# Performance work log

Measured on AMD Instinct MI355X. Metric: run time of the kernel, lower is better.

The kernel has to match this reference:

```python
import jax, jax.numpy as jnp
import numpy as np

B, F = 512, 300  # F must satisfy F+4 == 16*19
EPS = 1e-5

def _leaky(v):
    return jnp.where(v >= 0, v, 0.01 * v)

def setup_inputs() -> dict:
    key = jax.random.key(0)
    ks = jax.random.split(key, 9)
    def conv_w(k, o, i):
        return jax.random.normal(k, (o, i), dtype=jnp.float32) * (1.0 / np.sqrt(i))
    x = jax.random.uniform(ks[0], (B, F), dtype=jnp.float32)
    return {
        "x": x,
        "w1": conv_w(ks[1], 256, 512), "b1": jnp.zeros((256,), jnp.float32),
        "w2": conv_w(ks[2], 128, 256), "b2": jnp.zeros((128,), jnp.float32),
        "w3": conv_w(ks[3], 64, 128),  "b3": jnp.zeros((64,), jnp.float32),
        "w4": conv_w(ks[4], 4, 64),    "b4": jnp.zeros((4,), jnp.float32),
    }

def reference(x, w1, b1, w2, b2, w3, b3, w4, b4):
    b = x.shape[0]
    xp = jnp.pad(x, ((0, 0), (2, 2)))                       # (b, 304)
    s1 = xp[:, None, :]                                      # unsqueeze(1)
    s2 = xp[:, :, None]                                      # unsqueeze(2)
    DI = s1 - s2                                             # (b,304,304)
    NDI = DI / (s1 + s2 + EPS)
    t = jnp.stack([DI, NDI], axis=-1)                        # (b,304,304,2)
    # tile into 16x16 grid of 19x19 patches, concat patches along channel
    # channel c = (row*16+col)*2 + d  (row-major loop order in original)
    t = t.reshape(b, 16, 19, 16, 19, 2).transpose(0, 2, 4, 1, 3, 5).reshape(b, 19, 19, 512)
    h = _leaky(jnp.einsum('bhwc,oc->bhwo', t, w1) + b1)      # (b,19,19,256)
    h = _leaky(jnp.einsum('bhwc,oc->bhwo', h, w2) + b2)      # (b,19,19,128)
    # masking branch (positional encoding in original is dead code / overwritten)
    m = jax.nn.relu(jnp.einsum('bhwc,oc->bhwo', h, w3) + b3)  # (b,19,19,64)
    m = jax.nn.relu(jnp.einsum('bhwc,oc->bhwo', m, w4) + b4)  # (b,19,19,4)
    m = m.transpose(3, 0, 1, 2).reshape(4, b, 19 * 19)
    m = jax.nn.softmax(m, axis=2).reshape(4, b, 19, 19, 1)
    # split 128 channels into 4 groups of 32
    g = h.reshape(b, 19, 19, 4, 32).transpose(3, 0, 1, 2, 4)  # (4,b,19,19,32)
    out = (g * m).sum(axis=(2, 3))                            # (4,b,32)
    return out.transpose(1, 0, 2).reshape(b, 128)
```

## Files before the change

kernel.cpp:

```cpp
#include <hip/hip_runtime.h>
#include <math.h>

typedef unsigned short ushort_t;
typedef __attribute__((ext_vector_type(8))) short short8;
typedef __attribute__((ext_vector_type(4))) float f32x4;

#define NTILES 12

#define WS_W_USHORTS 115712

__device__ inline ushort_t f2bf(float f) {
    unsigned u = __float_as_uint(f);
    return (ushort_t)((u + 0x7FFFu + ((u >> 16) & 1u)) >> 16);
}
__device__ inline unsigned pkbf(float f0, float f1) {
    unsigned a = __float_as_uint(f0) + 0x8000u;
    unsigned b = __float_as_uint(f1) + 0x8000u;
    return __builtin_amdgcn_perm(b, a, 0x07060302u);
}
__device__ inline float leaky(float v) { return fmaxf(v, 0.01f * v); }

__global__ void pack_weights(const float* __restrict__ w1, const float* __restrict__ w2,
                             const float* __restrict__ w3, const float* __restrict__ w4,
                             ushort_t* __restrict__ ws) {
    const int idx = blockIdx.x * 256 + threadIdx.x;
    if (idx >= WS_W_USHORTS) return;
    float val = 0.f;
    if (idx < 73728) {
        const int j = idx & 7, lane = (idx >> 3) & 63, blk = idx >> 9;
        const int ks = blk % 9, os = blk / 9;
        const int m = lane & 15, q = lane >> 4;
        const int row = os * 16 + m;
        if (ks < 8) {
            const int k = ks * 32 + q * 8 + j;
            const int i1 = k >> 4, j1 = k & 15;
            val = w1[row * 512 + i1 * 32 + j1 * 2 + 1];
        } else {
            const int sub = q * 8 + j;
            if (sub < 16) {
                const int j1 = sub;
                float s = 0.f;
                #pragma unroll
                for (int i1 = 0; i1 < 16; ++i1) s += w1[row * 512 + i1 * 32 + j1 * 2];
                val = s;
            } else {
                const int i1 = sub - 16;
                float s = 0.f;
                #pragma unroll
                for (int j1 = 0; j1 < 16; ++j1) s += w1[row * 512 + i1 * 32 + j1 * 2];
                val = -s;
            }
        }
    } else if (idx < 106496) {
        const int l = idx - 73728;
        const int j = l & 7, lane = (l >> 3) & 63, blk = l >> 9;
        const int ks = blk & 7, os = blk >> 3;
        const int m = lane & 15, q = lane >> 4;
        val = w2[(os * 16 + m) * 256 + ks * 32 + q * 8 + j];
    } else if (idx < 114688) {
        const int l = idx - 106496;
        const int j = l & 7, lane = (l >> 3) & 63, blk = l >> 9;
        const int ks = blk & 3, os = blk >> 2;
        const int m = lane & 15, q = lane >> 4;
        val = w3[(os * 16 + m) * 128 + ks * 32 + q * 8 + j];
    } else {
        const int l = idx - 114688;
        const int j = l & 7, lane = (l >> 3) & 63, ks = l >> 9;
        const int m = lane & 15, q = lane >> 4;
        val = (m < 4) ? w4[m * 64 + ks * 32 + q * 8 + j] : 0.f;
    }
    ws[idx] = f2bf(val);
}

template <int NS>
__global__ __launch_bounds__(256, 3) void fused_mfma(
    const float* __restrict__ x, const ushort_t* __restrict__ ws,
    const float* __restrict__ b1, const float* __restrict__ b2,
    const float* __restrict__ b3, const float* __restrict__ b4,
    float* __restrict__ partA, float* __restrict__ partS)
{
    __shared__ __align__(16) ushort_t sm[19048];
    ushort_t* const ts   = sm;
    ushort_t* const h2s  = sm;
    ushort_t* const h1s  = sm + 10240;
    ushort_t* const m3s  = sm + 10240;
    float*   const ebuf  = (float*)(sm + 12288);
    float*   const xp    = (float*)(sm + 18432);

    constexpr int SH  = (NS == 4) ? 2 : ((NS == 2) ? 1 : 0);
    constexpr int TPS = (NTILES + NS - 1) / NS;
    const int tid = threadIdx.x;
    const int s   = blockIdx.x & (NS - 1);
    const int bb  = blockIdx.x >> SH;
    const int t0  = s * TPS;
    const int t1  = (t0 + TPS < NTILES) ? (t0 + TPS) : NTILES;

    const int wid  = tid >> 6;
    const int lane = tid & 63;
    const int n0   = lane & 15;
    const int qi   = lane >> 4;
    const int sx   = n0 & 7;
    const int row0 = qi * 4;

    for (int jj = tid; jj < 308; jj += 256) {
        float v = 0.f;
        const int src = jj - 2;
        if (src >= 0 && src < 300) v = x[bb * 300 + src];
        xp[jj] = v;
    }

    const short8* wf1 = (const short8*)(ws);
    const short8* wf2 = (const short8*)(ws + 73728);
    const short8* wf3 = (const short8*)(ws + 106496);
    const short8* wf4 = (const short8*)(ws + 114688);

    f32x4 bv1[4], bv2[2], bv3, bv4;
    #pragma unroll
    for (int jo = 0; jo < 4; ++jo) bv1[jo] = *(const f32x4*)&b1[(wid * 4 + jo) * 16 + row0];
    #pragma unroll
    for (int jo = 0; jo < 2; ++jo) bv2[jo] = *(const f32x4*)&b2[(wid * 2 + jo) * 16 + row0];
    bv3 = *(const f32x4*)&b3[wid * 16 + row0];
    bv4 = *(const f32x4*)&b4[0];

    f32x4 Afr[2] = {{0.f, 0.f, 0.f, 0.f}, {0.f, 0.f, 0.f, 0.f}};
    float Ss = 0.f;

    __syncthreads();

    for (int tile = t0; tile < t1; ++tile) {
        const int pos0 = tile * 32;

        {
            const int p   = tid & 31;
            const int i1b = tid >> 5;
            int posg = pos0 + p; if (posg > 360) posg = 360;
            const int hh = posg / 19;
            const int ww = posg - 19 * hh;
            const int base = p * 320;
            const int psw  = p & 7;
            float u[16];
            #pragma unroll
            for (int j1 = 0; j1 < 16; ++j1) u[j1] = xp[j1 * 19 + ww];
            #pragma unroll
            for (int ii = 0; ii < 2; ++ii) {
                const int i1 = i1b + ii * 8;
                const float v = xp[i1 * 19 + hh];
                #pragma unroll
                for (int j1 = 0; j1 < 16; j1 += 2) {
                    const float nd0 = (u[j1] - v)     * __builtin_amdgcn_rcpf(u[j1] + v + 1e-5f);
                    const float nd1 = (u[j1 + 1] - v) * __builtin_amdgcn_rcpf(u[j1 + 1] + v + 1e-5f);
                    const int oct = i1 * 2 + (j1 >> 3);
                    *(unsigned*)&ts[base + ((oct ^ psw) << 3) + (j1 & 7)] = pkbf(nd0, nd1);
                }
            }
            if (i1b == 0) {
                #pragma unroll
                for (int j1 = 0; j1 < 16; j1 += 2) {
                    const int oct = 32 + (j1 >> 3);
                    *(unsigned*)&ts[base + ((oct ^ psw) << 3) + (j1 & 7)] = pkbf(u[j1], u[j1 + 1]);
                }
                #pragma unroll
                for (int i1 = 0; i1 < 16; i1 += 2) {
                    const float v0 = xp[i1 * 19 + hh];
                    const float v1 = xp[(i1 + 1) * 19 + hh];
                    const int oct = 34 + (i1 >> 3);
                    *(unsigned*)&ts[base + ((oct ^ psw) << 3) + (i1 & 7)] = pkbf(v0, v1);
                }
            }
        }
        __syncthreads();

        {
            f32x4 acc[4][2];
            #pragma unroll
            for (int jo = 0; jo < 4; ++jo) { acc[jo][0] = bv1[jo]; acc[jo][1] = bv1[jo]; }
            const int tb0 = n0 * 320;
            const int tb1 = tb0 + 16 * 320;
            const int wbase = wid * 2304 + lane;
            #pragma unroll 3
            for (int ks = 0; ks < 9; ++ks) {
                const int oct = ks * 4 + qi;
                const short8 bb0 = *(const short8*)&ts[tb0 + ((oct ^ sx) << 3)];
                const short8 bb1 = *(const short8*)&ts[tb1 + ((oct ^ sx) << 3)];
                #pragma unroll
                for (int jo = 0; jo < 4; ++jo) {
                    const short8 a = wf1[wbase + (jo * 9 + ks) * 64];
                    acc[jo][0] = __builtin_amdgcn_mfma_f32_16x16x32_bf16(a, bb0, acc[jo][0], 0, 0, 0);
                    acc[jo][1] = __builtin_amdgcn_mfma_f32_16x16x32_bf16(a, bb1, acc[jo][1], 0, 0, 0);
                }
            }
            #pragma unroll
            for (int jo = 0; jo < 4; ++jo) {
                const int out0 = (wid * 4 + jo) * 16 + row0;
                #pragma unroll
                for (int ps = 0; ps < 2; ++ps) {
                    const f32x4 a4 = acc[jo][ps];
                    uint2 pk;
                    pk.x = pkbf(leaky(a4.x), leaky(a4.y));
                    pk.y = pkbf(leaky(a4.z), leaky(a4.w));
                    *(uint2*)&h1s[(ps * 16 + n0) * 256 + (((out0 >> 3) ^ sx) << 3) + (out0 & 7)] = pk;
                }
            }
        }
        __syncthreads();

        f32x4 h2f[2][2];
        {
            f32x4 acc[2][2];
            #pragma unroll
            for (int jo = 0; jo < 2; ++jo) { acc[jo][0] = bv2[jo]; acc[jo][1] = bv2[jo]; }
            const int hb0 = n0 * 256;
            const int hb1 = hb0 + 16 * 256;
            const int wbase = wid * 1024 + lane;
            #pragma unroll 4
            for (int ks = 0; ks < 8; ++ks) {
                const int oct = ks * 4 + qi;
                const short8 bb0 = *(const short8*)&h1s[hb0 + ((oct ^ sx) << 3)];
                const short8 bb1 = *(const short8*)&h1s[hb1 + ((oct ^ sx) << 3)];
                #pragma unroll
                for (int jo = 0; jo < 2; ++jo) {
                    const short8 a = wf2[wbase + (jo * 8 + ks) * 64];
                    acc[jo][0] = __builtin_amdgcn_mfma_f32_16x16x32_bf16(a, bb0, acc[jo][0], 0, 0, 0);
                    acc[jo][1] = __builtin_amdgcn_mfma_f32_16x16x32_bf16(a, bb1, acc[jo][1], 0, 0, 0);
                }
            }
            #pragma unroll
            for (int jo = 0; jo < 2; ++jo) {
                const int out0 = (wid * 2 + jo) * 16 + row0;
                #pragma unroll
                for (int ps = 0; ps < 2; ++ps) {
                    f32x4 a4 = acc[jo][ps];
                    a4.x = leaky(a4.x); a4.y = leaky(a4.y);
                    a4.z = leaky(a4.z); a4.w = leaky(a4.w);
                    h2f[jo][ps] = a4;
                    uint2 pk;
                    pk.x = pkbf(a4.x, a4.y);
                    pk.y = pkbf(a4.z, a4.w);
                    *(uint2*)&h2s[(ps * 16 + n0) * 128 + (((out0 >> 3) ^ sx) << 3) + (out0 & 7)] = pk;
                }
            }
        }
        __syncthreads();

        {
            f32x4 acc[2] = {bv3, bv3};
            const int cb0 = n0 * 128;
            const int cb1 = cb0 + 16 * 128;
            #pragma unroll
            for (int ks = 0; ks < 4; ++ks) {
                const int oct = ks * 4 + qi;
                const short8 bb0 = *(const short8*)&h2s[cb0 + ((oct ^ sx) << 3)];
                const short8 bb1 = *(const short8*)&h2s[cb1 + ((oct ^ sx) << 3)];
                const short8 a = wf3[(wid * 4 + ks) * 64 + lane];
                acc[0] = __builtin_amdgcn_mfma_f32_16x16x32_bf16(a, bb0, acc[0], 0, 0, 0);
                acc[1] = __builtin_amdgcn_mfma_f32_16x16x32_bf16(a, bb1, acc[1], 0, 0, 0);
            }
            const int out0 = wid * 16 + row0;
            #pragma unroll
            for (int ps = 0; ps < 2; ++ps) {
                const f32x4 a4 = acc[ps];
                uint2 pk;
                pk.x = pkbf(fmaxf(a4.x, 0.f), fmaxf(a4.y, 0.f));
                pk.y = pkbf(fmaxf(a4.z, 0.f), fmaxf(a4.w, 0.f));
                *(uint2*)&m3s[(ps * 16 + n0) * 64 + (((out0 >> 3) ^ sx) << 3) + (out0 & 7)] = pk;
            }
        }
        __syncthreads();

        if (wid == 0) {
            f32x4 acc[2] = {bv4, bv4};
            const int mb0 = n0 * 64;
            const int mb1 = mb0 + 16 * 64;
            #pragma unroll
            for (int ks = 0; ks < 2; ++ks) {
                const int oct = ks * 4 + qi;
                const short8 bb0 = *(const short8*)&m3s[mb0 + ((oct ^ sx) << 3)];
                const short8 bb1 = *(const short8*)&m3s[mb1 + ((oct ^ sx) << 3)];
                const short8 a = wf4[ks * 64 + lane];
                acc[0] = __builtin_amdgcn_mfma_f32_16x16x32_bf16(a, bb0, acc[0], 0, 0, 0);
                acc[1] = __builtin_amdgcn_mfma_f32_16x16x32_bf16(a, bb1, acc[1], 0, 0, 0);
            }
            if (lane < 16) {
                const bool bad0 = (pos0 + lane) > 360;
                const bool bad1 = (pos0 + 16 + lane) > 360;
                ebuf[0 * 32 + lane]      = bad0 ? 0.f : __expf(fmaxf(acc[0].x, 0.f));
                ebuf[1 * 32 + lane]      = bad0 ? 0.f : __expf(fmaxf(acc[0].y, 0.f));
                ebuf[2 * 32 + lane]      = bad0 ? 0.f : __expf(fmaxf(acc[0].z, 0.f));
                ebuf[3 * 32 + lane]      = bad0 ? 0.f : __expf(fmaxf(acc[0].w, 0.f));
                ebuf[0 * 32 + 16 + lane] = bad1 ? 0.f : __expf(fmaxf(acc[1].x, 0.f));
                ebuf[1 * 32 + 16 + lane] = bad1 ? 0.f : __expf(fmaxf(acc[1].y, 0.f));
                ebuf[2 * 32 + 16 + lane] = bad1 ? 0.f : __expf(fmaxf(acc[1].z, 0.f));
                ebuf[3 * 32 + 16 + lane] = bad1 ? 0.f : __expf(fmaxf(acc[1].w, 0.f));
            }
        }
        __syncthreads();

        {
            const float e0 = ebuf[wid * 32 + n0];
            const float e1 = ebuf[wid * 32 + 16 + n0];
            #pragma unroll
            for (int jo = 0; jo < 2; ++jo) {
                Afr[jo].x += e0 * h2f[jo][0].x + e1 * h2f[jo][1].x;
                Afr[jo].y += e0 * h2f[jo][0].y + e1 * h2f[jo][1].y;
                Afr[jo].z += e0 * h2f[jo][0].z + e1 * h2f[jo][1].z;
                Afr[jo].w += e0 * h2f[jo][0].w + e1 * h2f[jo][1].w;
            }
            Ss += e0 + e1;
        }
    }

    #pragma unroll
    for (int bit = 1; bit < 16; bit <<= 1) {
        #pragma unroll
        for (int jo = 0; jo < 2; ++jo) {
            Afr[jo].x += __shfl_xor(Afr[jo].x, bit, 64);
            Afr[jo].y += __shfl_xor(Afr[jo].y, bit, 64);
            Afr[jo].z += __shfl_xor(Afr[jo].z, bit, 64);
            Afr[jo].w += __shfl_xor(Afr[jo].w, bit, 64);
        }
        Ss += __shfl_xor(Ss, bit, 64);
    }
    if (n0 == 0) {
        const int pbA = (s * 512 + bb) * 128;
        #pragma unroll
        for (int jo = 0; jo < 2; ++jo) {
            const int ch0 = (wid * 2 + jo) * 16 + qi * 4;
            partA[pbA + ch0]     = Afr[jo].x;
            partA[pbA + ch0 + 1] = Afr[jo].y;
            partA[pbA + ch0 + 2] = Afr[jo].z;
            partA[pbA + ch0 + 3] = Afr[jo].w;
        }
        if (qi == 0) partS[(s * 512 + bb) * 4 + wid] = Ss;
    }
}

template <int NS>
__global__ void merge_out(const float* __restrict__ partA, const float* __restrict__ partS,
                          float* __restrict__ out) {
    const int idx = blockIdx.x * 256 + threadIdx.x;
    if (idx >= 512 * 128) return;
    const int bb = idx >> 7, ch = idx & 127;
    const int q = ch >> 5;
    float Sf = 0.f, Af = 0.f;
    #pragma unroll
    for (int s = 0; s < NS; ++s) {
        Af += partA[(s * 512 + bb) * 128 + ch];
        Sf += partS[(s * 512 + bb) * 4 + q];
    }
    out[idx] = Af / Sf;
}

__global__ __launch_bounds__(256, 2) void fallback_fused(
    const float* __restrict__ x,
    const float* __restrict__ w1, const float* __restrict__ b1,
    const float* __restrict__ w2, const float* __restrict__ b2,
    const float* __restrict__ w3, const float* __restrict__ b3,
    const float* __restrict__ w4, const float* __restrict__ b4,
    float* __restrict__ out)
{
    __shared__ float smf[14644];
    float* const xp  = smf;
    float* const ts  = smf + 308;
    float* const h1s = smf + 8500;
    float* const h2s = smf + 12596;
    float* const m3s = ts;
    float* const lgs = ts + 1024;

    const int tid = threadIdx.x;
    const int b   = blockIdx.x;
    for (int j = tid; j < 308; j += 256) {
        float v = 0.f;
        const int src = j - 2;
        if (src >= 0 && src < 300) v = x[b * 300 + src];
        xp[j] = v;
    }
    __syncthreads();
    const int q = tid >> 5, dd = tid & 31;
    float M = -1e30f, S = 0.f, A = 0.f;
    for (int tile = 0; tile < 23; ++tile) {
        const int pos0 = tile * 16;
        {
            const int p = tid & 15, kk0 = tid >> 4;
            const int pos = pos0 + p;
            const bool valid = (pos < 361);
            const int hh = valid ? (pos / 19) : 0;
            const int ww = valid ? (pos - hh * 19) : 0;
            #pragma unroll
            for (int i = 0; i < 16; ++i) {
                const int kk = kk0 + (i << 4);
                const int i1 = kk >> 4, j1 = kk & 15;
                float di = 0.f, ndi = 0.f;
                if (valid) {
                    const float u = xp[j1 * 19 + ww];
                    const float v = xp[i1 * 19 + hh];
                    di = u - v; ndi = di / (u + v + 1e-5f);
                }
                ts[(kk << 5) + p] = di;
                ts[(kk << 5) + 16 + p] = ndi;
            }
        }
        __syncthreads();
        {
            const int o = tid;
            float acc[16];
            const float bias = b1[o];
            #pragma unroll
            for (int p = 0; p < 16; ++p) acc[p] = bias;
            for (int k = 0; k < 512; ++k) {
                const float wv = w1[o * 512 + k];
                #pragma unroll
                for (int p = 0; p < 16; ++p) acc[p] += wv * ts[(k << 4) + p];
            }
            #pragma unroll
            for (int p = 0; p < 16; ++p) h1s[(o << 4) + p] = (acc[p] >= 0.f) ? acc[p] : 0.01f * acc[p];
        }
        __syncthreads();
        {
            const int o2 = tid & 127, pb = (tid >> 7) << 3;
            float acc[8];
            const float bias = b2[o2];
            #pragma unroll
            for (int j = 0; j < 8; ++j) acc[j] = bias;
            for (int k = 0; k < 256; ++k) {
                const float wv = w2[o2 * 256 + k];
                #pragma unroll
                for (int j = 0; j < 8; ++j) acc[j] += wv * h1s[(k << 4) + pb + j];
            }
            #pragma unroll
            for (int j = 0; j < 8; ++j) h2s[(o2 << 4) + pb + j] = (acc[j] >= 0.f) ? acc[j] : 0.01f * acc[j];
        }
        __syncthreads();
        {
            const int o3 = tid & 63, pb = (tid >> 6) << 2;
            float acc[4];
            const float bias = b3[o3];
            #pragma unroll
            for (int j = 0; j < 4; ++j) acc[j] = bias;
            for (int k = 0; k < 128; ++k) {
                const float wv = w3[o3 * 128 + k];
                #pragma unroll
                for (int j = 0; j < 4; ++j) acc[j] += wv * h2s[(k << 4) + pb + j];
            }
            #pragma unroll
            for (int j = 0; j < 4; ++j) m3s[(o3 << 4) + pb + j] = fmaxf(acc[j], 0.f);
        }
        __syncthreads();
        if (tid < 64) {
            const int o4 = tid >> 4, p = tid & 15;
            float a = b4[o4];
            for (int k = 0; k < 64; ++k) a += w4[o4 * 64 + k] * m3s[(k << 4) + p];
            a = fmaxf(a, 0.f);
            if (pos0 + p >= 361) a = -1e30f;
            lgs[(o4 << 4) + p] = a;
        }
        __syncthreads();
        if (tid < 128) {
            float l[16];
            #pragma unroll
            for (int p = 0; p < 16; ++p) l[p] = lgs[(q << 4) + p];
            float tmax = l[0];
            #pragma unroll
            for (int p = 1; p < 16; ++p) tmax = fmaxf(tmax, l[p]);
            const float newM = fmaxf(M, tmax);
            const float alpha = __expf(M - newM);
            float ssum = 0.f, asum = 0.f;
            #pragma unroll
            for (int p = 0; p < 16; ++p) {
                const float e = __expf(l[p] - newM);
                ssum += e;
                asum += e * h2s[(((q << 5) + dd) << 4) + p];
            }
            S = S * alpha + ssum; A = A * alpha + asum; M = newM;
        }
        __syncthreads();
    }
    if (tid < 128) out[(b << 7) + tid] = A / S;
}

extern "C" void kernel_launch(void* const* d_in, const int* in_sizes, int n_in,
                              void* d_out, int out_size, void* d_ws, size_t ws_size,
                              hipStream_t stream) {
    const float* x  = (const float*)d_in[0];
    const float* w1 = (const float*)d_in[1];
    const float* b1 = (const float*)d_in[2];
    const float* w2 = (const float*)d_in[3];
    const float* b2 = (const float*)d_in[4];
    const float* w3 = (const float*)d_in[5];
    const float* b3 = (const float*)d_in[6];
    const float* w4 = (const float*)d_in[7];
    const float* b4 = (const float*)d_in[8];
    float* out = (float*)d_out;

    const size_t wbytes = (size_t)WS_W_USHORTS * sizeof(ushort_t);
    ushort_t* ws = (ushort_t*)d_ws;
    const int packBlocks = (WS_W_USHORTS + 255) / 256;

    const size_t need4 = wbytes + (size_t)4 * 512 * 132 * sizeof(float);
    const size_t need2 = wbytes + (size_t)2 * 512 * 132 * sizeof(float);
    const size_t need1 = wbytes + (size_t)1 * 512 * 132 * sizeof(float);

    if (ws_size >= need4) {
        float* pA = (float*)((char*)d_ws + wbytes);
        float* pS = pA + (size_t)4 * 512 * 128;
        pack_weights<<<packBlocks, 256, 0, stream>>>(w1, w2, w3, w4, ws);
        fused_mfma<4><<<2048, 256, 0, stream>>>(x, ws, b1, b2, b3, b4, pA, pS);
        merge_out<4><<<256, 256, 0, stream>>>(pA, pS, out);
    } else if (ws_size >= need2) {
        float* pA = (float*)((char*)d_ws + wbytes);
        float* pS = pA + (size_t)2 * 512 * 128;
        pack_weights<<<packBlocks, 256, 0, stream>>>(w1, w2, w3, w4, ws);
        fused_mfma<2><<<1024, 256, 0, stream>>>(x, ws, b1, b2, b3, b4, pA, pS);
        merge_out<2><<<256, 256, 0, stream>>>(pA, pS, out);
    } else if (ws_size >= need1) {
        float* pA = (float*)((char*)d_ws + wbytes);
        float* pS = pA + (size_t)1 * 512 * 128;
        pack_weights<<<packBlocks, 256, 0, stream>>>(w1, w2, w3, w4, ws);
        fused_mfma<1><<<512, 256, 0, stream>>>(x, ws, b1, b2, b3, b4, pA, pS);
        merge_out<1><<<256, 256, 0, stream>>>(pA, pS, out);
    } else {
        fallback_fused<<<512, 256, 0, stream>>>(x, w1, b1, w2, b2, w3, b3, w4, b4, out);
    }
}
```

Measured before the change: 169.0 us.

## Fuse layer-4 projection into layer-3 epilogue, dropping a barrier and LDS round-trip

The 64->4 layer-4 projection now runs as a register dot product in the layer-3 MFMA epilogue. Each wave applies its slice of w4 (fp32, kept in registers), reduces across quad groups with shuffles, and writes partial logits to LDS. Each wave then sums the four partials for its own mask channel and applies relu and exp. This removes the bf16 staging of m3, a single-wave MFMA stage and one __syncthreads per tile. Layer-3 weights are also hoisted into registers outside the tile loop, which raises register pressure under launch_bounds(256,3).

Result: no change. 168.7 us (-0.2%).

```diff
diff --git a/kernel.cpp b/kernel.cpp
--- a/kernel.cpp
+++ b/kernel.cpp
@@ -7,7 +7,7 @@
 
 #define NTILES 12
 
-#define WS_W_USHORTS 115712
+#define WS_W_USHORTS 114688
 
 __device__ inline ushort_t f2bf(float f) {
     unsigned u = __float_as_uint(f);
@@ -21,8 +21,7 @@
 __device__ inline float leaky(float v) { return fmaxf(v, 0.01f * v); }
 
 __global__ void pack_weights(const float* __restrict__ w1, const float* __restrict__ w2,
-                             const float* __restrict__ w3, const float* __restrict__ w4,
-                             ushort_t* __restrict__ ws) {
+                             const float* __restrict__ w3, ushort_t* __restrict__ ws) {
     const int idx = blockIdx.x * 256 + threadIdx.x;
     if (idx >= WS_W_USHORTS) return;
     float val = 0.f;
@@ -57,17 +56,12 @@
         const int ks = blk & 7, os = blk >> 3;
         const int m = lane & 15, q = lane >> 4;
         val = w2[(os * 16 + m) * 256 + ks * 32 + q * 8 + j];
-    } else if (idx < 114688) {
+    } else {
         const int l = idx - 106496;
         const int j = l & 7, lane = (l >> 3) & 63, blk = l >> 9;
         const int ks = blk & 3, os = blk >> 2;
         const int m = lane & 15, q = lane >> 4;
         val = w3[(os * 16 + m) * 128 + ks * 32 + q * 8 + j];
-    } else {
-        const int l = idx - 114688;
-        const int j = l & 7, lane = (l >> 3) & 63, ks = l >> 9;
-        const int m = lane & 15, q = lane >> 4;
-        val = (m < 4) ? w4[m * 64 + ks * 32 + q * 8 + j] : 0.f;
     }
     ws[idx] = f2bf(val);
 }
@@ -77,14 +71,14 @@
     const float* __restrict__ x, const ushort_t* __restrict__ ws,
     const float* __restrict__ b1, const float* __restrict__ b2,
     const float* __restrict__ b3, const float* __restrict__ b4,
+    const float* __restrict__ w4,
     float* __restrict__ partA, float* __restrict__ partS)
 {
     __shared__ __align__(16) ushort_t sm[19048];
     ushort_t* const ts   = sm;
     ushort_t* const h2s  = sm;
     ushort_t* const h1s  = sm + 10240;
-    ushort_t* const m3s  = sm + 10240;
-    float*   const ebuf  = (float*)(sm + 12288);
+    float*   const wbuf  = (float*)(sm + 10240);
     float*   const xp    = (float*)(sm + 18432);
 
     constexpr int SH  = (NS == 4) ? 2 : ((NS == 2) ? 1 : 0);
@@ -112,15 +106,20 @@
     const short8* wf1 = (const short8*)(ws);
     const short8* wf2 = (const short8*)(ws + 73728);
     const short8* wf3 = (const short8*)(ws + 106496);
-    const short8* wf4 = (const short8*)(ws + 114688);
-
-    f32x4 bv1[4], bv2[2], bv3, bv4;
+
+    f32x4 bv1[4], bv2[2], bv3;
     #pragma unroll
     for (int jo = 0; jo < 4; ++jo) bv1[jo] = *(const f32x4*)&b1[(wid * 4 + jo) * 16 + row0];
     #pragma unroll
     for (int jo = 0; jo < 2; ++jo) bv2[jo] = *(const f32x4*)&b2[(wid * 2 + jo) * 16 + row0];
     bv3 = *(const f32x4*)&b3[wid * 16 + row0];
-    bv4 = *(const f32x4*)&b4[0];
+    short8 wr3[4];
+    #pragma unroll
+    for (int ks = 0; ks < 4; ++ks) wr3[ks] = wf3[(wid * 4 + ks) * 64 + lane];
+    f32x4 w4r[4];
+    #pragma unroll
+    for (int q = 0; q < 4; ++q) w4r[q] = *(const f32x4*)&w4[q * 64 + wid * 16 + row0];
+    const float b4s = b4[wid];
 
     f32x4 Afr[2] = {{0.f, 0.f, 0.f, 0.f}, {0.f, 0.f, 0.f, 0.f}};
     float Ss = 0.f;
@@ -251,61 +250,49 @@
                 const int oct = ks * 4 + qi;
                 const short8 bb0 = *(const short8*)&h2s[cb0 + ((oct ^ sx) << 3)];
                 const short8 bb1 = *(const short8*)&h2s[cb1 + ((oct ^ sx) << 3)];
-                const short8 a = wf3[(wid * 4 + ks) * 64 + lane];
-                acc[0] = __builtin_amdgcn_mfma_f32_16x16x32_bf16(a, bb0, acc[0], 0, 0, 0);
-                acc[1] = __builtin_amdgcn_mfma_f32_16x16x32_bf16(a, bb1, acc[1], 0, 0, 0);
-            }
-            const int out0 = wid * 16 + row0;
+                acc[0] = __builtin_amdgcn_mfma_f32_16x16x32_bf16(wr3[ks], bb0, acc[0], 0, 0, 0);
+                acc[1] = __builtin_amdgcn_mfma_f32_16x16x32_bf16(wr3[ks], bb1, acc[1], 0, 0, 0);
+            }
             #pragma unroll
             for (int ps = 0; ps < 2; ++ps) {
-                const f32x4 a4 = acc[ps];
-                uint2 pk;
-                pk.x = pkbf(fmaxf(a4.x, 0.f), fmaxf(a4.y, 0.f));
-                pk.y = pkbf(fmaxf(a4.z, 0.f), fmaxf(a4.w, 0.f));
-                *(uint2*)&m3s[(ps * 16 + n0) * 64 + (((out0 >> 3) ^ sx) << 3) + (out0 & 7)] = pk;
-            }
-        }
-        __syncthreads();
-
-        if (wid == 0) {
-            f32x4 acc[2] = {bv4, bv4};
-            const int mb0 = n0 * 64;
-            const int mb1 = mb0 + 16 * 64;
-            #pragma unroll
-            for (int ks = 0; ks < 2; ++ks) {
-                const int oct = ks * 4 + qi;
-                const short8 bb0 = *(const short8*)&m3s[mb0 + ((oct ^ sx) << 3)];
-                const short8 bb1 = *(const short8*)&m3s[mb1 + ((oct ^ sx) << 3)];
-                const short8 a = wf4[ks * 64 + lane];
-                acc[0] = __builtin_amdgcn_mfma_f32_16x16x32_bf16(a, bb0, acc[0], 0, 0, 0);
-                acc[1] = __builtin_amdgcn_mfma_f32_16x16x32_bf16(a, bb1, acc[1], 0, 0, 0);
-            }
-            if (lane < 16) {
-                const bool bad0 = (pos0 + lane) > 360;
-                const bool bad1 = (pos0 + 16 + lane) > 360;
-                ebuf[0 * 32 + lane]      = bad0 ? 0.f : __expf(fmaxf(acc[0].x, 0.f));
-                ebuf[1 * 32 + lane]      = bad0 ? 0.f : __expf(fmaxf(acc[0].y, 0.f));
-                ebuf[2 * 32 + lane]      = bad0 ? 0.f : __expf(fmaxf(acc[0].z, 0.f));
-                ebuf[3 * 32 + lane]      = bad0 ? 0.f : __expf(fmaxf(acc[0].w, 0.f));
-                ebuf[0 * 32 + 16 + lane] = bad1 ? 0.f : __expf(fmaxf(acc[1].x, 0.f));
-                ebuf[1 * 32 + 16 + lane] = bad1 ? 0.f : __expf(fmaxf(acc[1].y, 0.f));
-                ebuf[2 * 32 + 16 + lane] = bad1 ? 0.f : __expf(fmaxf(acc[1].z, 0.f));
-                ebuf[3 * 32 + 16 + lane] = bad1 ? 0.f : __expf(fmaxf(acc[1].w, 0.f));
-            }
-        }
-        __syncthreads();
-
-        {
-            const float e0 = ebuf[wid * 32 + n0];
-            const float e1 = ebuf[wid * 32 + 16 + n0];
-            #pragma unroll
-            for (int jo = 0; jo < 2; ++jo) {
-                Afr[jo].x += e0 * h2f[jo][0].x + e1 * h2f[jo][1].x;
-                Afr[jo].y += e0 * h2f[jo][0].y + e1 * h2f[jo][1].y;
-                Afr[jo].z += e0 * h2f[jo][0].z + e1 * h2f[jo][1].z;
-                Afr[jo].w += e0 * h2f[jo][0].w + e1 * h2f[jo][1].w;
-            }
-            Ss += e0 + e1;
+                f32x4 m3 = acc[ps];
+                m3.x = fmaxf(m3.x, 0.f); m3.y = fmaxf(m3.y, 0.f);
+                m3.z = fmaxf(m3.z, 0.f); m3.w = fmaxf(m3.w, 0.f);
+                float pl[4];
+                #pragma unroll
+                for (int q = 0; q < 4; ++q)
+                    pl[q] = w4r[q].x * m3.x + w4r[q].y * m3.y + w4r[q].z * m3.z + w4r[q].w * m3.w;
+                #pragma unroll
+                for (int q = 0; q < 4; ++q) {
+                    pl[q] += __shfl_xor(pl[q], 16, 64);
+                    pl[q] += __shfl_xor(pl[q], 32, 64);
+                }
+                if (qi == 0) {
+                    #pragma unroll
+                    for (int q = 0; q < 4; ++q)
+                        wbuf[(wid * 4 + q) * 32 + ps * 16 + n0] = pl[q];
+                }
+            }
+        }
+        __syncthreads();
+
+        {
+            #pragma unroll
+            for (int ps = 0; ps < 2; ++ps) {
+                const int pos = ps * 16 + n0;
+                float lg = wbuf[(0 * 4 + wid) * 32 + pos] + wbuf[(1 * 4 + wid) * 32 + pos]
+                         + wbuf[(2 * 4 + wid) * 32 + pos] + wbuf[(3 * 4 + wid) * 32 + pos] + b4s;
+                lg = fmaxf(lg, 0.f);
+                const float e = ((pos0 + pos) > 360) ? 0.f : __expf(lg);
+                #pragma unroll
+                for (int jo = 0; jo < 2; ++jo) {
+                    Afr[jo].x += e * h2f[jo][ps].x;
+                    Afr[jo].y += e * h2f[jo][ps].y;
+                    Afr[jo].z += e * h2f[jo][ps].z;
+                    Afr[jo].w += e * h2f[jo][ps].w;
+                }
+                Ss += e;
+            }
         }
     }
 
@@ -502,20 +489,20 @@
     if (ws_size >= need4) {
         float* pA = (float*)((char*)d_ws + wbytes);
         float* pS = pA + (size_t)4 * 512 * 128;
-        pack_weights<<<packBlocks, 256, 0, stream>>>(w1, w2, w3, w4, ws);
-        fused_mfma<4><<<2048, 256, 0, stream>>>(x, ws, b1, b2, b3, b4, pA, pS);
+        pack_weights<<<packBlocks, 256, 0, stream>>>(w1, w2, w3, ws);
+        fused_mfma<4><<<2048, 256, 0, stream>>>(x, ws, b1, b2, b3, b4, w4, pA, pS);
         merge_out<4><<<256, 256, 0, stream>>>(pA, pS, out);
     } else if (ws_size >= need2) {
         float* pA = (float*)((char*)d_ws + wbytes);
         float* pS = pA + (size_t)2 * 512 * 128;
-        pack_weights<<<packBlocks, 256, 0, stream>>>(w1, w2, w3, w4, ws);
-        fused_mfma<2><<<1024, 256, 0, stream>>>(x, ws, b1, b2, b3, b4, pA, pS);
+        pack_weights<<<packBlocks, 256, 0, stream>>>(w1, w2, w3, ws);
+        fused_mfma<2><<<1024, 256, 0, stream>>>(x, ws, b1, b2, b3, b4, w4, pA, pS);
         merge_out<2><<<256, 256, 0, stream>>>(pA, pS, out);
     } else if (ws_size >= need1) {
         float* pA = (float*)((char*)d_ws + wbytes);
         float* pS = pA + (size_t)1 * 512 * 128;
-        pack_weights<<<packBlocks, 256, 0, stream>>>(w1, w2, w3, w4, ws);
-        fused_mfma<1><<<512, 256, 0, stream>>>(x, ws, b1, b2, b3, b4, pA, pS);
+        pack_weights<<<packBlocks, 256, 0, stream>>>(w1, w2, w3, ws);
+        fused_mfma<1><<<512, 256, 0, stream>>>(x, ws, b1, b2, b3, b4, w4, pA, pS);
         merge_out<1><<<256, 256, 0, stream>>>(pA, pS, out);
     } else {
         fallback_fused<<<512, 256, 0, stream>>>(x, w1, b1, w2, b2, w3, b3, w4, b4, out);
```
